# Kernel tuning notes

Hardware: AMD Instinct MI355X
Metric: run time of the kernel (lower is better)

The kernel has to match this reference:

```python
import jax, jax.numpy as jnp
import numpy as np
from jax import lax

N = 512      # input_dim (encoder feats)
B = 128      # num_feats (bottleneck)
H = 512      # num_hidden
K = 3        # kernel_size
X = 8        # num_layers per stack
R = 3        # num_stacks
L = X * R    # 24 conv blocks
NSRC = 2
BATCH = 8
T = 3200
EPS = 1e-8


def _gln(x, g, b):
    # GroupNorm(num_groups=1): normalize over (C, T) per sample; x: [B, C, T]
    mean = jnp.mean(x, axis=(1, 2), keepdims=True)
    var = jnp.mean(jnp.square(x - mean), axis=(1, 2), keepdims=True)
    return g[:, None] * (x - mean) * lax.rsqrt(var + EPS) + b[:, None]


def _prelu(x, a):
    return jnp.where(x >= 0, x, a * x)


def _pw(x, W, b):
    # pointwise (1x1) conv: x [B, Cin, T], W [Cout, Cin], b [Cout]
    return jnp.einsum('bct,oc->bot', x, W) + b[:, None]


def _dwconv(x, W, b, dil):
    # depthwise dilated conv, 'same' length (pad = dil for K=3): W [H, K]
    out = lax.conv_general_dilated(
        x, W[:, None, :], window_strides=(1,), padding=[(dil, dil)],
        rhs_dilation=(dil,), dimension_numbers=('NCH', 'OIH', 'NCH'),
        feature_group_count=H)
    return out + b[:, None]


def setup_inputs() -> dict:
    key = jax.random.key(0)
    ks = jax.random.split(key, 12)
    s = 0.02
    inp = {
        'x': jax.random.normal(ks[0], (BATCH, N, T), jnp.float32),
        'in_g': jnp.ones((N,), jnp.float32),
        'in_b': jnp.zeros((N,), jnp.float32),
        'Wc': jax.random.normal(ks[1], (B, N), jnp.float32) * s,
        'bc': jnp.zeros((B,), jnp.float32),
        'W1': jax.random.normal(ks[2], (L, H, B), jnp.float32) * s,
        'b1': jnp.zeros((L, H), jnp.float32),
        'a1': jnp.full((L,), 0.25, jnp.float32),
        'g1': jnp.ones((L, H), jnp.float32),
        'be1': jnp.zeros((L, H), jnp.float32),
        'Wd': jax.random.normal(ks[3], (L, H, K), jnp.float32) * s,
        'bd': jnp.zeros((L, H), jnp.float32),
        'a2': jnp.full((L,), 0.25, jnp.float32),
        'g2': jnp.ones((L, H), jnp.float32),
        'be2': jnp.zeros((L, H), jnp.float32),
        'Wres': jax.random.normal(ks[4], (L, B, H), jnp.float32) * s,
        'bres': jnp.zeros((L, B), jnp.float32),
        'Wskip': jax.random.normal(ks[5], (L, B, H), jnp.float32) * s,
        'bskip': jnp.zeros((L, B), jnp.float32),
        'a_out': jnp.asarray(0.25, jnp.float32),
        'Wo': jax.random.normal(ks[6], (NSRC * N, B), jnp.float32) * s,
        'bo': jnp.zeros((NSRC * N,), jnp.float32),
    }
    return inp


def reference(x, in_g, in_b, Wc, bc, W1, b1, a1, g1, be1, Wd, bd, a2, g2, be2,
              Wres, bres, Wskip, bskip, a_out, Wo, bo):
    feats = _gln(x, in_g, in_b)            # input GroupNorm(1, N)
    feats = _pw(feats, Wc, bc)             # [B, Bfeat, T]
    output = jnp.zeros_like(feats)
    for i in range(L):
        dil = 2 ** (i % X)
        h = _pw(feats, W1[i], b1[i])                 # 1x1: B -> H
        h = _gln(_prelu(h, a1[i]), g1[i], be1[i])
        h = _dwconv(h, Wd[i], bd[i], dil)            # depthwise dilated
        h = _gln(_prelu(h, a2[i]), g2[i], be2[i])
        output = output + _pw(h, Wskip[i], bskip[i])
        if i < L - 1:                                # last block: no residual
            feats = feats + _pw(h, Wres[i], bres[i])
    out = _prelu(output, a_out)
    out = _pw(out, Wo, bo)                 # [B, NSRC*N, T]
    out = jax.nn.sigmoid(out)
    return out.reshape(x.shape[0], NSRC, N, -1)
```

## Files before the change

kernel.cpp:

```cpp
#include <hip/hip_runtime.h>
#include <cstdint>
#include <cstddef>

#define BATCHN 8
#define TLEN   3200
#define NCH    512
#define BCH    128
#define HCH    512
#define LBLK   24
#define CNTF   (512.0f * 3200.0f)
#define EPSV   1e-8f
#define NSLOT  32

typedef float  floatx4 __attribute__((ext_vector_type(4)));
typedef short  short8  __attribute__((ext_vector_type(8)));
typedef short  short4v __attribute__((ext_vector_type(4)));

enum { EP_FIRST = 1, EP_LAST = 2 };

__device__ inline unsigned short f2bf(float f) {
    unsigned int u = __float_as_uint(f);
    u = (u + 0x7fffu + ((u >> 16) & 1u)) >> 16;
    return (unsigned short)u;
}
__device__ inline float bf2f(short s) {
    return __uint_as_float(((unsigned int)(unsigned short)s) << 16);
}

__device__ inline void gload_lds16(const unsigned short* g, unsigned short* l) {
    __builtin_amdgcn_global_load_lds(
        (const __attribute__((address_space(1))) unsigned int*)(g),
        (__attribute__((address_space(3))) unsigned int*)(l),
        16, 0, 0);
}

__device__ inline void block_reduce_atomic2(float s, float ss, float* out) {
#pragma unroll
    for (int off = 32; off; off >>= 1) {
        s  += __shfl_down(s, off, 64);
        ss += __shfl_down(ss, off, 64);
    }
    __shared__ float pr[8];
    const int wave = threadIdx.x >> 6;
    const int lane = threadIdx.x & 63;
    if (lane == 0) { pr[wave * 2] = s; pr[wave * 2 + 1] = ss; }
    __syncthreads();
    if (threadIdx.x == 0) {
        const int nw = blockDim.x >> 6;
        float a = 0.f, b = 0.f;
        for (int i = 0; i < nw; i++) { a += pr[i * 2]; b += pr[i * 2 + 1]; }
        atomicAdd(out, a);
        atomicAdd(out + 1, b);
    }
}

__device__ inline void load_stats32(const float* __restrict__ st,
                                    float& mu, float& rstd) {
    float s = 0.f, ss = 0.f;
#pragma unroll
    for (int i = 0; i < NSLOT; i++) { s += st[2 * i]; ss += st[2 * i + 1]; }
    mu = s * (1.f / CNTF);
    const float var = ss * (1.f / CNTF) - mu * mu;
    rstd = rsqrtf(var + EPSV);
}

template <int KDIM, int EP>
__global__ __launch_bounds__(256, 4) void mm_k(
    const unsigned short* __restrict__ X,
    const unsigned short* __restrict__ W,
    const float* __restrict__ bias, const float* __restrict__ uv,
    float* __restrict__ O_f32, unsigned short* __restrict__ O_bf,
    const float* __restrict__ outAcc_ro,
    const float* __restrict__ statsIn,
    const float* __restrict__ alphaPtr, int Cout)
{
    const int b    = blockIdx.z;
    const int t0   = blockIdx.x * 128;
    const int m0   = blockIdx.y * 128;
    const int lane = threadIdx.x & 63;
    const int wid  = threadIdx.x >> 6;
    const int wt   = wid & 1;
    const int wm   = wid >> 1;
    const int l15  = lane & 15;
    const int quad = lane >> 4;

    const unsigned short* Xb =
        X + ((size_t)b * TLEN + t0 + wt * 64 + l15) * KDIM + quad * 8;
    const unsigned short* Wb =
        W + (size_t)(m0 + wm * 64 + l15) * KDIM + quad * 8;

    floatx4 acc[4][4];
#pragma unroll
    for (int i = 0; i < 4; i++)
#pragma unroll
        for (int j = 0; j < 4; j++)
#pragma unroll
            for (int r = 0; r < 4; r++) acc[i][j][r] = 0.f;

#pragma unroll 2
    for (int kc = 0; kc < KDIM / 32; ++kc) {
        const int ko = kc * 32;
        short8 a[4], w[4];
#pragma unroll
        for (int i = 0; i < 4; i++)
            a[i] = *reinterpret_cast<const short8*>(Xb + (size_t)i * 16 * KDIM + ko);
#pragma unroll
        for (int j = 0; j < 4; j++)
            w[j] = *reinterpret_cast<const short8*>(Wb + (size_t)j * 16 * KDIM + ko);
#pragma unroll
        for (int i = 0; i < 4; i++)
#pragma unroll
            for (int j = 0; j < 4; j++)
                acc[i][j] = __builtin_amdgcn_mfma_f32_16x16x32_bf16(
                    w[j], a[i], acc[i][j], 0, 0, 0);
    }

    float mu = 0.f, rstd = 1.f, alpha = 0.f;
    load_stats32(statsIn + b * (2 * NSLOT), mu, rstd);
    if (EP == EP_LAST) alpha = alphaPtr[0];

#pragma unroll
    for (int j = 0; j < 4; j++) {
        const int cb = m0 + wm * 64 + j * 16 + quad * 4;
        const float4 b4 = *reinterpret_cast<const float4*>(bias + cb);
        const float4 u4 = *reinterpret_cast<const float4*>(uv + cb);
        const float4 v4 = *reinterpret_cast<const float4*>(
            uv + cb + (EP == EP_LAST ? 2 * BCH : Cout));
        float rb[4] = { b4.x + u4.x - mu * rstd * v4.x,
                        b4.y + u4.y - mu * rstd * v4.y,
                        b4.z + u4.z - mu * rstd * v4.z,
                        b4.w + u4.w - mu * rstd * v4.w };
#pragma unroll
        for (int i = 0; i < 4; i++) {
            const int t = t0 + wt * 64 + i * 16 + l15;
            const size_t idx = ((size_t)b * TLEN + t) * Cout + cb;
            if (EP == EP_FIRST) {
                float4 o;
                short4v s;
#pragma unroll
                for (int r = 0; r < 4; r++) {
                    const float val = rstd * acc[i][j][r] + rb[r];
                    (&o.x)[r] = val;
                    s[r] = (short)f2bf(val);
                }
                *reinterpret_cast<float4*>(O_f32 + idx) = o;
                *reinterpret_cast<short4v*>(O_bf + idx) = s;
            } else {
                const float4 oa = *reinterpret_cast<const float4*>(outAcc_ro + idx);
                short4v s;
#pragma unroll
                for (int r = 0; r < 4; r++) {
                    const float val = rstd * acc[i][j][r] + rb[r];
                    const float f = (&oa.x)[r] + val;
                    const float pv = f >= 0.f ? f : alpha * f;
                    s[r] = (short)f2bf(pv);
                }
                *reinterpret_cast<short4v*>(O_bf + idx) = s;
            }
        }
    }
}

__global__ __launch_bounds__(256, 4) void mm_h_lds_k(
    const unsigned short* __restrict__ X,
    const unsigned short* __restrict__ W,
    const float* __restrict__ bias,
    float* __restrict__ statsOut,
    const float* __restrict__ alphaPtr,
    unsigned short* __restrict__ O_bf)
{
    __shared__ unsigned short As[128 * 128];
    const int b    = blockIdx.z;
    const int t0   = blockIdx.x * 128;
    const int m0   = blockIdx.y * 128;
    const int lane = threadIdx.x & 63;
    const int wid  = threadIdx.x >> 6;
    const int wt   = wid & 1;
    const int wm   = wid >> 1;
    const int l15  = lane & 15;
    const int quad = lane >> 4;

#pragma unroll
    for (int q = 0; q < 8; q++) {
        const int r = wid * 32 + q * 4 + quad;
        const unsigned short* src =
            X + ((size_t)b * TLEN + t0 + r) * BCH + ((l15 ^ (r & 15)) * 8);
        gload_lds16(src, As + (wid * 32 + q * 4) * BCH);
    }
    __syncthreads();

    const unsigned short* Wb =
        W + (size_t)(m0 + wm * 64 + l15) * BCH + quad * 8;

    floatx4 acc[4][4];
#pragma unroll
    for (int i = 0; i < 4; i++)
#pragma unroll
        for (int j = 0; j < 4; j++)
#pragma unroll
            for (int r = 0; r < 4; r++) acc[i][j][r] = 0.f;

#pragma unroll
    for (int kc = 0; kc < 4; ++kc) {
        short8 a[4], w[4];
#pragma unroll
        for (int j = 0; j < 4; j++)
            w[j] = *reinterpret_cast<const short8*>(
                Wb + (size_t)j * 16 * BCH + kc * 32);
#pragma unroll
        for (int i = 0; i < 4; i++) {
            const int R  = wt * 64 + i * 16 + l15;
            const int sl = (kc * 4 + quad) ^ l15;
            a[i] = *reinterpret_cast<const short8*>(As + R * BCH + sl * 8);
        }
#pragma unroll
        for (int i = 0; i < 4; i++)
#pragma unroll
            for (int j = 0; j < 4; j++)
                acc[i][j] = __builtin_amdgcn_mfma_f32_16x16x32_bf16(
                    w[j], a[i], acc[i][j], 0, 0, 0);
    }

    const float alpha = alphaPtr[0];
    float ssum = 0.f, ssq = 0.f;
#pragma unroll
    for (int j = 0; j < 4; j++) {
        const int cb = m0 + wm * 64 + j * 16 + quad * 4;
        const float4 b4 = *reinterpret_cast<const float4*>(bias + cb);
#pragma unroll
        for (int i = 0; i < 4; i++) {
            const int t = t0 + wt * 64 + i * 16 + l15;
            short4v s;
#pragma unroll
            for (int r = 0; r < 4; r++) {
                float val = acc[i][j][r] + (&b4.x)[r];
                val = val >= 0.f ? val : alpha * val;
                ssum += val; ssq += val * val;
                s[r] = (short)f2bf(val);
            }
            *reinterpret_cast<short4v*>(
                O_bf + ((size_t)b * TLEN + t) * HCH + cb) = s;
        }
    }
    block_reduce_atomic2(ssum, ssq,
        statsOut + b * (2 * NSLOT) +
        ((blockIdx.x + blockIdx.y * 25) & (NSLOT - 1)) * 2);
}

__global__ __launch_bounds__(256, 2) void mm_dual_lds_k(
    const unsigned short* __restrict__ X,
    const unsigned short* __restrict__ Wsr,
    const float* __restrict__ bskip, const float* __restrict__ bres,
    const float* __restrict__ uv,
    float* __restrict__ feats, unsigned short* __restrict__ feats_bf,
    float* __restrict__ outAcc,
    const float* __restrict__ statsIn)
{
    __shared__ unsigned short As[2][64 * 128];
    const int b    = blockIdx.z;
    const int t0   = blockIdx.x * 64;
    const int lane = threadIdx.x & 63;
    const int wm   = threadIdx.x >> 6;
    const int l15  = lane & 15;
    const int quad = lane >> 4;

    const unsigned short* Wb =
        Wsr + (size_t)(wm * 64 + l15) * HCH + quad * 8;

    floatx4 acc[4][4];
#pragma unroll
    for (int i = 0; i < 4; i++)
#pragma unroll
        for (int j = 0; j < 4; j++)
#pragma unroll
            for (int r = 0; r < 4; r++) acc[i][j][r] = 0.f;

    const int srow = wm * 16;
#define STAGE_CHUNK(KC, BUF)                                                  \
    {                                                                         \
        _Pragma("unroll")                                                     \
        for (int q = 0; q < 4; q++) {                                         \
            const int r = srow + q * 4 + quad;                                \
            const unsigned short* src =                                       \
                X + ((size_t)b * TLEN + t0 + r) * HCH + (KC) * 128 +          \
                ((l15 ^ (r & 15)) * 8);                                       \
            gload_lds16(src, As[BUF] + (srow + q * 4) * 128);                 \
        }                                                                     \
    }

    STAGE_CHUNK(0, 0);
    __syncthreads();

#pragma unroll
    for (int kc = 0; kc < 4; ++kc) {
        if (kc < 3) STAGE_CHUNK(kc + 1, (kc + 1) & 1);
        const unsigned short* Ab = As[kc & 1];
#pragma unroll
        for (int ks = 0; ks < 4; ++ks) {
            short8 a[4], w[4];
#pragma unroll
            for (int j = 0; j < 4; j++)
                w[j] = *reinterpret_cast<const short8*>(
                    Wb + (size_t)j * 16 * HCH + kc * 128 + ks * 32);
#pragma unroll
            for (int i = 0; i < 4; i++) {
                const int R  = i * 16 + l15;
                const int sl = (ks * 4 + quad) ^ l15;
                a[i] = *reinterpret_cast<const short8*>(Ab + R * 128 + sl * 8);
            }
#pragma unroll
            for (int i = 0; i < 4; i++)
#pragma unroll
                for (int j = 0; j < 4; j++)
                    acc[i][j] = __builtin_amdgcn_mfma_f32_16x16x32_bf16(
                        w[j], a[i], acc[i][j], 0, 0, 0);
        }
        __syncthreads();
    }
#undef STAGE_CHUNK

    float mu, rstd;
    load_stats32(statsIn + b * (2 * NSLOT), mu, rstd);

    const bool sk = (wm < 2);
#pragma unroll
    for (int j = 0; j < 4; j++) {
        const int c  = wm * 64 + j * 16 + quad * 4;
        const int cc = sk ? c : c - 128;
        const float4 b4 = sk
            ? *reinterpret_cast<const float4*>(bskip + cc)
            : *reinterpret_cast<const float4*>(bres + cc);
        const float4 u4 = *reinterpret_cast<const float4*>(uv + c);
        const float4 v4 = *reinterpret_cast<const float4*>(uv + c + 256);
        float rb[4] = { b4.x + u4.x - mu * rstd * v4.x,
                        b4.y + u4.y - mu * rstd * v4.y,
                        b4.z + u4.z - mu * rstd * v4.z,
                        b4.w + u4.w - mu * rstd * v4.w };
#pragma unroll
        for (int i = 0; i < 4; i++) {
            const int t = t0 + i * 16 + l15;
            const size_t idx = ((size_t)b * TLEN + t) * BCH + cc;
            if (sk) {
                float4 oa = *reinterpret_cast<const float4*>(outAcc + idx);
#pragma unroll
                for (int r = 0; r < 4; r++)
                    (&oa.x)[r] += rstd * acc[i][j][r] + rb[r];
                *reinterpret_cast<float4*>(outAcc + idx) = oa;
            } else {
                float4 f = *reinterpret_cast<const float4*>(feats + idx);
                short4v s;
#pragma unroll
                for (int r = 0; r < 4; r++) {
                    (&f.x)[r] += rstd * acc[i][j][r] + rb[r];
                    s[r] = (short)f2bf((&f.x)[r]);
                }
                *reinterpret_cast<float4*>(feats + idx) = f;
                *reinterpret_cast<short4v*>(feats_bf + idx) = s;
            }
        }
    }
}

__global__ __launch_bounds__(256, 4) void mm_final_k(
    const unsigned short* __restrict__ Xbf, const unsigned short* __restrict__ Wb,
    const float* __restrict__ bo, float* __restrict__ out)
{
    const int b    = blockIdx.z;
    const int t0   = blockIdx.x * 128;
    const int m0   = blockIdx.y * 128;
    const int lane = threadIdx.x & 63;
    const int wid  = threadIdx.x >> 6;
    const int wc   = wid & 1;
    const int wr   = wid >> 1;
    const int l15  = lane & 15;
    const int quad = lane >> 4;

    const unsigned short* Wp =
        Wb + (size_t)(m0 + wr * 64 + l15) * BCH + quad * 8;
    const unsigned short* Xp =
        Xbf + ((size_t)b * TLEN + t0 + wc * 64 + l15) * BCH + quad * 8;

    floatx4 acc[4][4];
#pragma unroll
    for (int i = 0; i < 4; i++)
#pragma unroll
        for (int j = 0; j < 4; j++)
#pragma unroll
            for (int r = 0; r < 4; r++) acc[i][j][r] = 0.f;

#pragma unroll 2
    for (int kc = 0; kc < BCH / 32; ++kc) {
        const int ko = kc * 32;
        short8 a[4], x[4];
#pragma unroll
        for (int i = 0; i < 4; i++)
            a[i] = *reinterpret_cast<const short8*>(Wp + (size_t)i * 16 * BCH + ko);
#pragma unroll
        for (int j = 0; j < 4; j++)
            x[j] = *reinterpret_cast<const short8*>(Xp + (size_t)j * 16 * BCH + ko);
#pragma unroll
        for (int i = 0; i < 4; i++)
#pragma unroll
            for (int j = 0; j < 4; j++)
                acc[i][j] = __builtin_amdgcn_mfma_f32_16x16x32_bf16(
                    a[i], x[j], acc[i][j], 0, 0, 0);
    }

#pragma unroll
    for (int i = 0; i < 4; i++) {
        const int mb = m0 + wr * 64 + i * 16 + quad * 4;
#pragma unroll
        for (int r = 0; r < 4; r++) {
            const int m = mb + r;
            const float bz = bo[m];
#pragma unroll
            for (int j = 0; j < 4; j++) {
                const int t = t0 + wc * 64 + j * 16 + l15;
                const float val = acc[i][j][r] + bz;
                const float e = __expf(-val);
                out[((size_t)b * (2 * NCH) + m) * TLEN + t] =
                    __builtin_amdgcn_rcpf(1.f + e);
            }
        }
    }
}

__global__ __launch_bounds__(256) void prep_w_k(
    const float* __restrict__ W, const float* __restrict__ g,
    const float* __restrict__ be, unsigned short* __restrict__ Wout,
    float* __restrict__ uv, int Mrows, int K, int nmat, int Mout, int rowOff)
{
    const int r    = blockIdx.x * 4 + (threadIdx.x >> 6);
    const int lane = threadIdx.x & 63;
    if (r >= Mrows * nmat) return;
    const int mat = r / Mrows;
    const int m   = r - mat * Mrows;
    const float* Wrow = W + (size_t)r * K;
    const float* gv = g  ? g  + (size_t)mat * K : nullptr;
    const float* bv = be ? be + (size_t)mat * K : nullptr;
    unsigned short* orow = Wout + ((size_t)mat * Mout + rowOff + m) * K;
    float u = 0.f, v = 0.f;
    for (int k = lane * 4; k < K; k += 256) {
        float4 w4 = *reinterpret_cast<const float4*>(Wrow + k);
        float4 o4 = w4;
        if (gv) {
            const float4 g4 = *reinterpret_cast<const float4*>(gv + k);
            const float4 b4 = *reinterpret_cast<const float4*>(bv + k);
            o4.x = w4.x * g4.x; o4.y = w4.y * g4.y;
            o4.z = w4.z * g4.z; o4.w = w4.w * g4.w;
            u += w4.x * b4.x + w4.y * b4.y + w4.z * b4.z + w4.w * b4.w;
            v += w4.x * g4.x + w4.y * g4.y + w4.z * g4.z + w4.w * g4.w;
        }
        short4v s;
        s[0] = (short)f2bf(o4.x); s[1] = (short)f2bf(o4.y);
        s[2] = (short)f2bf(o4.z); s[3] = (short)f2bf(o4.w);
        *reinterpret_cast<short4v*>(orow + k) = s;
    }
    if (gv && uv) {
#pragma unroll
        for (int off = 32; off; off >>= 1) {
            u += __shfl_down(u, off, 64);
            v += __shfl_down(v, off, 64);
        }
        if (lane == 0) {
            uv[(size_t)mat * 2 * Mout + rowOff + m]        = u;
            uv[(size_t)mat * 2 * Mout + Mout + rowOff + m] = v;
        }
    }
}

__global__ __launch_bounds__(256) void tr_x_k(
    const float* __restrict__ x, unsigned short* __restrict__ xt,
    float* __restrict__ statsOut)
{
    __shared__ unsigned short tile[32][33];
    const int b  = blockIdx.z;
    const int t0 = blockIdx.x * 32;
    const int c0 = blockIdx.y * 32;
    const int tx = threadIdx.x & 31;
    const int ty = threadIdx.x >> 5;

    float s = 0.f, ss = 0.f;
#pragma unroll
    for (int r = 0; r < 4; r++) {
        const int cl = ty + r * 8;
        const float v = x[((size_t)b * NCH + c0 + cl) * TLEN + t0 + tx];
        s += v; ss += v * v;
        tile[tx][cl] = f2bf(v);
    }
    __syncthreads();
#pragma unroll
    for (int r = 0; r < 4; r++) {
        const int tl = ty + r * 8;
        xt[((size_t)b * TLEN + t0 + tl) * NCH + c0 + tx] = tile[tl][tx];
    }
    block_reduce_atomic2(s, ss,
        statsOut + b * (2 * NSLOT) +
        ((blockIdx.x + blockIdx.y * 25) & (NSLOT - 1)) * 2);
}

__global__ __launch_bounds__(256) void dwconv_k(
    const unsigned short* __restrict__ h, unsigned short* __restrict__ hd,
    const float* __restrict__ Wd, const float* __restrict__ bd,
    const float* __restrict__ g1, const float* __restrict__ be1,
    const float* __restrict__ statsIn, float* __restrict__ statsOut,
    const float* __restrict__ a2p, int dil)
{
    const int b  = blockIdx.y;
    const int tb = blockIdx.x * 16 + (threadIdx.x >> 6) * 4;
    const int c0 = (threadIdx.x & 63) * 8;

    float mu, rstd;
    load_stats32(statsIn + b * (2 * NSLOT), mu, rstd);
    const float alpha = a2p[0];

    float g[8], be[8], bz[8], wall[24];
#pragma unroll
    for (int q = 0; q < 6; q++) {
        const float4 w4 = *reinterpret_cast<const float4*>(Wd + (size_t)c0 * 3 + q * 4);
        wall[q * 4 + 0] = w4.x; wall[q * 4 + 1] = w4.y;
        wall[q * 4 + 2] = w4.z; wall[q * 4 + 3] = w4.w;
    }
    {
        const float4 ga = *reinterpret_cast<const float4*>(g1 + c0);
        const float4 gb = *reinterpret_cast<const float4*>(g1 + c0 + 4);
        const float4 ba = *reinterpret_cast<const float4*>(be1 + c0);
        const float4 bb = *reinterpret_cast<const float4*>(be1 + c0 + 4);
        const float4 da = *reinterpret_cast<const float4*>(bd + c0);
        const float4 db = *reinterpret_cast<const float4*>(bd + c0 + 4);
        const float gg[8] = { ga.x, ga.y, ga.z, ga.w, gb.x, gb.y, gb.z, gb.w };
        const float bbv[8] = { ba.x, ba.y, ba.z, ba.w, bb.x, bb.y, bb.z, bb.w };
        const float dd[8] = { da.x, da.y, da.z, da.w, db.x, db.y, db.z, db.w };
#pragma unroll
        for (int jj = 0; jj < 8; jj++) {
            g[jj]  = gg[jj] * rstd;
            be[jj] = bbv[jj] - mu * rstd * gg[jj];
            bz[jj] = dd[jj];
        }
    }

    float psum = 0.f, psq = 0.f;
#pragma unroll
    for (int it = 0; it < 4; ++it) {
        const int t = tb + it;
        const size_t rowb = ((size_t)b * TLEN + t) * HCH + c0;
        const bool hasP = (t - dil) >= 0;
        const bool hasN = (t + dil) < TLEN;
        const short8 cur = *reinterpret_cast<const short8*>(h + rowb);
        short8 prv = {}, nxt = {};
        if (hasP) prv = *reinterpret_cast<const short8*>(h + rowb - (size_t)dil * HCH);
        if (hasN) nxt = *reinterpret_cast<const short8*>(h + rowb + (size_t)dil * HCH);

        short8 o;
#pragma unroll
        for (int jj = 0; jj < 8; jj++) {
            float acc = bz[jj] + wall[jj * 3 + 1] * (g[jj] * bf2f(cur[jj]) + be[jj]);
            if (hasP) acc += wall[jj * 3 + 0] * (g[jj] * bf2f(prv[jj]) + be[jj]);
            if (hasN) acc += wall[jj * 3 + 2] * (g[jj] * bf2f(nxt[jj]) + be[jj]);
            const float v = acc >= 0.f ? acc : alpha * acc;
            o[jj] = (short)f2bf(v);
            psum += v; psq += v * v;
        }
        *reinterpret_cast<short8*>(hd + rowb) = o;
    }
    block_reduce_atomic2(psum, psq,
        statsOut + b * (2 * NSLOT) + (blockIdx.x & (NSLOT - 1)) * 2);
}

extern "C" void kernel_launch(void* const* d_in, const int* in_sizes, int n_in,
                              void* d_out, int out_size, void* d_ws, size_t ws_size,
                              hipStream_t stream)
{
    (void)in_sizes; (void)n_in; (void)out_size; (void)ws_size;

    const float* x    = (const float*)d_in[0];
    const float* in_g = (const float*)d_in[1];
    const float* in_b = (const float*)d_in[2];
    const float* Wc   = (const float*)d_in[3];
    const float* bc   = (const float*)d_in[4];
    const float* W1   = (const float*)d_in[5];
    const float* b1   = (const float*)d_in[6];
    const float* a1   = (const float*)d_in[7];
    const float* g1   = (const float*)d_in[8];
    const float* be1  = (const float*)d_in[9];
    const float* Wd   = (const float*)d_in[10];
    const float* bd   = (const float*)d_in[11];
    const float* a2   = (const float*)d_in[12];
    const float* g2   = (const float*)d_in[13];
    const float* be2  = (const float*)d_in[14];
    const float* Wres = (const float*)d_in[15];
    const float* bres = (const float*)d_in[16];
    const float* Wskip= (const float*)d_in[17];
    const float* bskip= (const float*)d_in[18];
    const float* aout = (const float*)d_in[19];
    const float* Wo   = (const float*)d_in[20];
    const float* bo   = (const float*)d_in[21];
    float* out = (float*)d_out;

    uint8_t* p = (uint8_t*)d_ws;
    unsigned short* x_t      = (unsigned short*)p; p += (size_t)BATCHN*TLEN*NCH*2;
    float*          feats    = (float*)p;          p += (size_t)BATCHN*TLEN*BCH*4;
    unsigned short* feats_bf = (unsigned short*)p; p += (size_t)BATCHN*TLEN*BCH*2;
    float*          outAcc   = (float*)p;          p += (size_t)BATCHN*TLEN*BCH*4;
    unsigned short* h        = (unsigned short*)p; p += (size_t)BATCHN*TLEN*HCH*2;
    unsigned short* hd       = (unsigned short*)p; p += (size_t)BATCHN*TLEN*HCH*2;
    unsigned short* WcG      = (unsigned short*)p; p += (size_t)BCH*NCH*2;
    unsigned short* W1b      = (unsigned short*)p; p += (size_t)LBLK*HCH*BCH*2;
    unsigned short* Wsr      = (unsigned short*)p; p += (size_t)LBLK*256*HCH*2;
    unsigned short* Wob      = (unsigned short*)p; p += (size_t)(2*NCH)*BCH*2;
    float*          uv_c     = (float*)p;          p += (size_t)2*BCH*4;
    float*          uv_sr    = (float*)p;          p += (size_t)LBLK*2*256*4;
    float*          stats    = (float*)p;

    const size_t SLOTF = (size_t)BATCHN * 2 * NSLOT;

    hipMemsetAsync(stats, 0, (size_t)49 * SLOTF * sizeof(float), stream);
    hipMemsetAsync(outAcc, 0, (size_t)BATCHN*TLEN*BCH*sizeof(float), stream);

    tr_x_k<<<dim3(100, 16, BATCHN), 256, 0, stream>>>(x, x_t, stats);
    prep_w_k<<<32,   256, 0, stream>>>(Wc,   in_g,    in_b,    WcG, uv_c, BCH,   NCH, 1,      BCH, 0);
    prep_w_k<<<3072, 256, 0, stream>>>(W1,   nullptr, nullptr, W1b, nullptr, HCH, BCH, LBLK,  HCH, 0);
    prep_w_k<<<768,  256, 0, stream>>>(Wskip,g2,      be2,     Wsr, uv_sr, BCH,  HCH, LBLK,   256, 0);
    prep_w_k<<<736,  256, 0, stream>>>(Wres, g2,      be2,     Wsr, uv_sr, BCH,  HCH, LBLK-1, 256, 128);
    prep_w_k<<<256,  256, 0, stream>>>(Wo,   nullptr, nullptr, Wob, nullptr, 2*NCH, BCH, 1,   2*NCH, 0);

    mm_k<NCH, EP_FIRST><<<dim3(25, 1, BATCHN), 256, 0, stream>>>(
        x_t, WcG, bc, uv_c, feats, feats_bf, nullptr, stats, nullptr, BCH);

    for (int i = 0; i < LBLK; i++) {
        float* st_h  = stats + (size_t)(1 + 2 * i) * SLOTF;
        float* st_hd = stats + (size_t)(2 + 2 * i) * SLOTF;
        const int dil = 1 << (i & 7);

        mm_h_lds_k<<<dim3(25, 4, BATCHN), 256, 0, stream>>>(
            feats_bf, W1b + (size_t)i * HCH * BCH,
            b1 + (size_t)i * HCH, st_h, a1 + i, h);

        dwconv_k<<<dim3(TLEN / 16, BATCHN), 256, 0, stream>>>(
            h, hd, Wd + (size_t)i * HCH * 3, bd + (size_t)i * HCH,
            g1 + (size_t)i * HCH, be1 + (size_t)i * HCH,
            st_h, st_hd, a2 + i, dil);

        if (i < LBLK - 1) {
            mm_dual_lds_k<<<dim3(50, 1, BATCHN), 256, 0, stream>>>(
                hd, Wsr + (size_t)i * 256 * HCH,
                bskip + (size_t)i * BCH, bres + (size_t)i * BCH,
                uv_sr + (size_t)i * 2 * 256,
                feats, feats_bf, outAcc, st_hd);
        } else {
            mm_k<HCH, EP_LAST><<<dim3(25, 1, BATCHN), 256, 0, stream>>>(
                hd, Wsr + (size_t)i * 256 * HCH,
                bskip + (size_t)i * BCH, uv_sr + (size_t)i * 2 * 256,
                nullptr, feats_bf, outAcc, st_hd, aout, BCH);
        }
    }

    mm_final_k<<<dim3(25, 8, BATCHN), 256, 0, stream>>>(
        feats_bf, Wob, bo, out);
}
```

Before: 1.940 ms.

## Fuse next block's bottleneck-to-hidden matmul into residual/skip matmul epilogue

The residual/skip kernel now keeps its updated bf16 feature tile in LDS and immediately runs the next block's 1x1 conv (W1) on it, applying bias and PReLU and accumulating the GroupNorm statistics. The standalone W1 kernel now runs only once, before the loop. This removes 23 kernel launches and the global write and re-read of the bf16 feature copy. In exchange, the fused kernel runs on 400 blocks instead of 800 for the hidden matmul and does more work per block, which can cost latency hiding and raise register pressure. It also reuses the LDS staging buffer, which needs correct synchronisation.

```diff
diff --git a/kernel.cpp b/kernel.cpp
--- a/kernel.cpp
+++ b/kernel.cpp
@@ -247,14 +247,19 @@
         ((blockIdx.x + blockIdx.y * 25) & (NSLOT - 1)) * 2);
 }
 
-__global__ __launch_bounds__(256, 2) void mm_dual_lds_k(
+__global__ __launch_bounds__(256, 2) void mm_dual_h_k(
     const unsigned short* __restrict__ X,
     const unsigned short* __restrict__ Wsr,
     const float* __restrict__ bskip, const float* __restrict__ bres,
     const float* __restrict__ uv,
-    float* __restrict__ feats, unsigned short* __restrict__ feats_bf,
+    float* __restrict__ feats,
     float* __restrict__ outAcc,
-    const float* __restrict__ statsIn)
+    const float* __restrict__ statsIn,
+    const unsigned short* __restrict__ W1,
+    const float* __restrict__ b1,
+    const float* __restrict__ a1p,
+    float* __restrict__ statsOut,
+    unsigned short* __restrict__ h_out)
 {
     __shared__ unsigned short As[2][64 * 128];
     const int b    = blockIdx.z;
@@ -355,10 +360,74 @@
                     s[r] = (short)f2bf((&f.x)[r]);
                 }
                 *reinterpret_cast<float4*>(feats + idx) = f;
-                *reinterpret_cast<short4v*>(feats_bf + idx) = s;
+                const int row = i * 16 + l15;
+                const int sl  = (cc >> 3) ^ l15;
+                *reinterpret_cast<short4v*>(
+                    As[0] + row * 128 + sl * 8 + (cc & 7)) = s;
             }
         }
     }
+    __syncthreads();
+
+    const float alpha1 = a1p[0];
+    float ssum = 0.f, ssq = 0.f;
+#pragma unroll
+    for (int mc = 0; mc < 2; ++mc) {
+        const int mb = wm * 128 + mc * 64;
+        const unsigned short* W1p =
+            W1 + (size_t)(mb + l15) * BCH + quad * 8;
+
+        floatx4 acc2[4][4];
+#pragma unroll
+        for (int i = 0; i < 4; i++)
+#pragma unroll
+            for (int j = 0; j < 4; j++)
+#pragma unroll
+                for (int r = 0; r < 4; r++) acc2[i][j][r] = 0.f;
+
+#pragma unroll
+        for (int kc = 0; kc < 4; ++kc) {
+            short8 a[4], w[4];
+#pragma unroll
+            for (int j = 0; j < 4; j++)
+                w[j] = *reinterpret_cast<const short8*>(
+                    W1p + (size_t)j * 16 * BCH + kc * 32);
+#pragma unroll
+            for (int i = 0; i < 4; i++) {
+                const int R  = i * 16 + l15;
+                const int sl = (kc * 4 + quad) ^ l15;
+                a[i] = *reinterpret_cast<const short8*>(As[0] + R * 128 + sl * 8);
+            }
+#pragma unroll
+            for (int i = 0; i < 4; i++)
+#pragma unroll
+                for (int j = 0; j < 4; j++)
+                    acc2[i][j] = __builtin_amdgcn_mfma_f32_16x16x32_bf16(
+                        w[j], a[i], acc2[i][j], 0, 0, 0);
+        }
+
+#pragma unroll
+        for (int j = 0; j < 4; j++) {
+            const int cb = mb + j * 16 + quad * 4;
+            const float4 b4 = *reinterpret_cast<const float4*>(b1 + cb);
+#pragma unroll
+            for (int i = 0; i < 4; i++) {
+                const int t = t0 + i * 16 + l15;
+                short4v s;
+#pragma unroll
+                for (int r = 0; r < 4; r++) {
+                    float val = acc2[i][j][r] + (&b4.x)[r];
+                    val = val >= 0.f ? val : alpha1 * val;
+                    ssum += val; ssq += val * val;
+                    s[r] = (short)f2bf(val);
+                }
+                *reinterpret_cast<short4v*>(
+                    h_out + ((size_t)b * TLEN + t) * HCH + cb) = s;
+            }
+        }
+    }
+    block_reduce_atomic2(ssum, ssq,
+        statsOut + b * (2 * NSLOT) + (blockIdx.x & (NSLOT - 1)) * 2);
 }
 
 __global__ __launch_bounds__(256, 4) void mm_final_k(
@@ -627,26 +696,28 @@
     mm_k<NCH, EP_FIRST><<<dim3(25, 1, BATCHN), 256, 0, stream>>>(
         x_t, WcG, bc, uv_c, feats, feats_bf, nullptr, stats, nullptr, BCH);
 
+    mm_h_lds_k<<<dim3(25, 4, BATCHN), 256, 0, stream>>>(
+        feats_bf, W1b, b1, stats + SLOTF, a1, h);
+
     for (int i = 0; i < LBLK; i++) {
         float* st_h  = stats + (size_t)(1 + 2 * i) * SLOTF;
         float* st_hd = stats + (size_t)(2 + 2 * i) * SLOTF;
         const int dil = 1 << (i & 7);
 
-        mm_h_lds_k<<<dim3(25, 4, BATCHN), 256, 0, stream>>>(
-            feats_bf, W1b + (size_t)i * HCH * BCH,
-            b1 + (size_t)i * HCH, st_h, a1 + i, h);
-
         dwconv_k<<<dim3(TLEN / 16, BATCHN), 256, 0, stream>>>(
             h, hd, Wd + (size_t)i * HCH * 3, bd + (size_t)i * HCH,
             g1 + (size_t)i * HCH, be1 + (size_t)i * HCH,
             st_h, st_hd, a2 + i, dil);
 
         if (i < LBLK - 1) {
-            mm_dual_lds_k<<<dim3(50, 1, BATCHN), 256, 0, stream>>>(
+            mm_dual_h_k<<<dim3(50, 1, BATCHN), 256, 0, stream>>>(
                 hd, Wsr + (size_t)i * 256 * HCH,
                 bskip + (size_t)i * BCH, bres + (size_t)i * BCH,
                 uv_sr + (size_t)i * 2 * 256,
-                feats, feats_bf, outAcc, st_hd);
+                feats, outAcc, st_hd,
+                W1b + (size_t)(i + 1) * HCH * BCH,
+                b1 + (size_t)(i + 1) * HCH, a1 + (i + 1),
+                stats + (size_t)(1 + 2 * (i + 1)) * SLOTF, h);
         } else {
             mm_k<HCH, EP_LAST><<<dim3(25, 1, BATCHN), 256, 0, stream>>>(
                 hd, Wsr + (size_t)i * 256 * HCH,
```

New measurement: 1.752 ms. -9.7%, faster.
